# Performance work log

Measured on AMD Instinct MI355X. Metric: run time of the kernel, lower is better.

## Reference

```python
import jax, jax.numpy as jnp
import numpy as np

Q = 10000   # num_question
D = 64      # dim_s
M = 50      # size_m
B = 64      # batch
T = 512     # seq_len


def setup_inputs() -> dict:
    key = jax.random.key(0)
    ks = jax.random.split(key, 14)
    s = 1.0 / np.sqrt(D)
    inp = {
        "question": jax.random.randint(ks[0], (B, T), 0, Q, dtype=jnp.int32),
        "response": jax.random.randint(ks[1], (B, T), 0, 2, dtype=jnp.int32),
        "mask": jnp.ones((B, T), dtype=jnp.float32),
        "k_emb": jax.random.normal(ks[2], (Q, D), jnp.float32) * s,
        "v_emb": jax.random.normal(ks[3], (2 * Q, D), jnp.float32) * s,
        "Mk": jax.random.normal(ks[4], (M, D), jnp.float32) * np.sqrt(2.0 / D),
        "Mv0": jax.random.normal(ks[5], (M, D), jnp.float32) * np.sqrt(2.0 / D),
        "e_W": jax.random.normal(ks[6], (D, D), jnp.float32) * s,
        "e_b": jnp.zeros((D,), jnp.float32),
        "a_W": jax.random.normal(ks[7], (D, D), jnp.float32) * s,
        "a_b": jnp.zeros((D,), jnp.float32),
        "f_W": jax.random.normal(ks[8], (2 * D, D), jnp.float32) * (1.0 / np.sqrt(2 * D)),
        "f_b": jnp.zeros((D,), jnp.float32),
        "p_W": jax.random.normal(ks[9], (D, 1), jnp.float32) * s,
        "p_b": jnp.zeros((1,), jnp.float32),
    }
    return inp


def reference(question, response, mask, k_emb, v_emb, Mk, Mv0,
              e_W, e_b, a_W, a_b, f_W, f_b, p_W, p_b):
    num_q = k_emb.shape[0]
    bsz = question.shape[0]
    x = question + num_q * response                      # [B,T] combined ids
    k = k_emb[question]                                  # [B,T,D]
    v = v_emb[x]                                         # [B,T,D]
    w = jax.nn.softmax(k @ Mk.T, axis=-1)                # [B,T,M] read/write weights
    e = jax.nn.sigmoid(v @ e_W + e_b)                    # [B,T,D] erase
    a = jnp.tanh(v @ a_W + a_b)                          # [B,T,D] add

    def step(Mvt, inp):
        wt, et, at, mt = inp                             # [B,M],[B,D],[B,D],[B]
        Mvn = Mvt * (1.0 - wt[:, :, None] * et[:, None, :]) + wt[:, :, None] * at[:, None, :]
        Mvt = jnp.where(mt[:, None, None] == 1, Mvn, Mvt)
        return Mvt, Mvt

    Mv0b = jnp.broadcast_to(Mv0, (bsz,) + Mv0.shape)     # [B,M,D]
    xs = (jnp.swapaxes(w, 0, 1), jnp.swapaxes(e, 0, 1),
          jnp.swapaxes(a, 0, 1), mask.T)
    _, Mv_seq = jax.lax.scan(step, Mv0b, xs)             # [T,B,M,D] states after steps 0..T-1
    # read at step t (t>=1) uses state after step t-1
    Mv_read = jnp.swapaxes(Mv_seq[:-1], 0, 1)            # [B,T-1,M,D]
    read = jnp.einsum('btm,btmd->btd', w[:, 1:], Mv_read)
    f = jnp.tanh(jnp.concatenate([read, k[:, 1:]], axis=-1) @ f_W + f_b)
    p = (f @ p_W + p_b).squeeze(-1)                      # [B,T-1]
    return p
```

## Files before the change

kernel.cpp:

```cpp
#include <hip/hip_runtime.h>
#include <cstddef>

#define QN 10000
#define DD 64
#define MM 50
#define BB 64
#define TT 512
#define WPAD 52
#define MG 25

#define PIN(arr, n)                                        \
  _Pragma("unroll") for (int _p = 0; _p < (n); ++_p)       \
      asm volatile("" : "+v"((arr)[_p]));

__global__ __launch_bounds__(256) void kPre(
    const int* __restrict__ question, const int* __restrict__ response,
    const float* __restrict__ mask,
    const float* __restrict__ k_emb, const float* __restrict__ v_emb,
    const float* __restrict__ Mk,
    const float* __restrict__ e_W, const float* __restrict__ e_b,
    const float* __restrict__ a_W, const float* __restrict__ a_b,
    float* __restrict__ w_buf, float* __restrict__ e_buf,
    float* __restrict__ a_buf) {
  const int lane = (int)(threadIdx.x & 63);
  const int wslot = __builtin_amdgcn_readfirstlane((int)(threadIdx.x >> 6));
  const int gw = blockIdx.x * 4 + wslot;
  const int NW = gridDim.x * 4;
  const int third = NW / 3;
  if (gw >= 3 * third) return;
  const int role = gw / third;
  const int idx = gw - role * third;
  const int stride4 = third * 4;

  if (role == 0) {
    float mk[64];
    const int mrow = lane < MM ? lane : (MM - 1);
#pragma unroll
    for (int i = 0; i < 64; i += 4) {
      const float4 t4 = *(const float4*)(Mk + mrow * 64 + i);
      mk[i] = t4.x; mk[i + 1] = t4.y; mk[i + 2] = t4.z; mk[i + 3] = t4.w;
    }
    for (int base = idx * 4; base < BB * TT; base += stride4) {
      const int4 q4 = *(const int4*)(question + base);
      const float* __restrict__ kr0 = k_emb + (size_t)q4.x * 64;
      const float* __restrict__ kr1 = k_emb + (size_t)q4.y * 64;
      const float* __restrict__ kr2 = k_emb + (size_t)q4.z * 64;
      const float* __restrict__ kr3 = k_emb + (size_t)q4.w * 64;
      float l00=0.f,l01=0.f,l02=0.f,l03=0.f;
      float l10=0.f,l11=0.f,l12=0.f,l13=0.f;
      float l20=0.f,l21=0.f,l22=0.f,l23=0.f;
      float l30=0.f,l31=0.f,l32=0.f,l33=0.f;
#pragma unroll
      for (int i = 0; i < 64; i += 4) {
        const float4 k0 = *(const float4*)(kr0 + i);
        const float4 k1 = *(const float4*)(kr1 + i);
        const float4 k2 = *(const float4*)(kr2 + i);
        const float4 k3 = *(const float4*)(kr3 + i);
        l00 = fmaf(k0.x, mk[i], l00); l01 = fmaf(k0.y, mk[i+1], l01);
        l02 = fmaf(k0.z, mk[i+2], l02); l03 = fmaf(k0.w, mk[i+3], l03);
        l10 = fmaf(k1.x, mk[i], l10); l11 = fmaf(k1.y, mk[i+1], l11);
        l12 = fmaf(k1.z, mk[i+2], l12); l13 = fmaf(k1.w, mk[i+3], l13);
        l20 = fmaf(k2.x, mk[i], l20); l21 = fmaf(k2.y, mk[i+1], l21);
        l22 = fmaf(k2.z, mk[i+2], l22); l23 = fmaf(k2.w, mk[i+3], l23);
        l30 = fmaf(k3.x, mk[i], l30); l31 = fmaf(k3.y, mk[i+1], l31);
        l32 = fmaf(k3.z, mk[i+2], l32); l33 = fmaf(k3.w, mk[i+3], l33);
      }
      float lm[4];
      lm[0] = (l00 + l01) + (l02 + l03);
      lm[1] = (l10 + l11) + (l12 + l13);
      lm[2] = (l20 + l21) + (l22 + l23);
      lm[3] = (l30 + l31) + (l32 + l33);
#pragma unroll
      for (int r = 0; r < 4; ++r) {
        float lv = (lane < MM) ? lm[r] : -3.4e38f;
#pragma unroll
        for (int off = 32; off > 0; off >>= 1) lv = fmaxf(lv, __shfl_xor(lv, off));
        float pe = (lane < MM) ? __expf(lm[r] - lv) : 0.f;
        float ss = pe;
#pragma unroll
        for (int off = 32; off > 0; off >>= 1) ss += __shfl_xor(ss, off);
        if (lane < MM) w_buf[(size_t)(base + r) * WPAD + lane] = pe / ss;
      }
    }
  } else if (role == 1) {
    float ew[64];
#pragma unroll
    for (int i = 0; i < 64; ++i) ew[i] = e_W[i * 64 + lane];
    const float eb = e_b[lane];
    for (int base = idx * 4; base < BB * TT; base += stride4) {
      const int4 q4 = *(const int4*)(question + base);
      const int4 r4 = *(const int4*)(response + base);
      const float4 m4 = *(const float4*)(mask + base);
      const float* __restrict__ v0 = v_emb + ((size_t)q4.x + (size_t)QN * r4.x) * 64;
      const float* __restrict__ v1 = v_emb + ((size_t)q4.y + (size_t)QN * r4.y) * 64;
      const float* __restrict__ v2 = v_emb + ((size_t)q4.z + (size_t)QN * r4.z) * 64;
      const float* __restrict__ v3 = v_emb + ((size_t)q4.w + (size_t)QN * r4.w) * 64;
      float e00 = eb, e01 = 0.f, e10 = eb, e11 = 0.f;
      float e20 = eb, e21 = 0.f, e30 = eb, e31 = 0.f;
#pragma unroll
      for (int i = 0; i < 64; i += 2) {
        const float2 a0 = *(const float2*)(v0 + i);
        const float2 a1 = *(const float2*)(v1 + i);
        const float2 a2 = *(const float2*)(v2 + i);
        const float2 a3 = *(const float2*)(v3 + i);
        e00 = fmaf(a0.x, ew[i], e00); e01 = fmaf(a0.y, ew[i+1], e01);
        e10 = fmaf(a1.x, ew[i], e10); e11 = fmaf(a1.y, ew[i+1], e11);
        e20 = fmaf(a2.x, ew[i], e20); e21 = fmaf(a2.y, ew[i+1], e21);
        e30 = fmaf(a3.x, ew[i], e30); e31 = fmaf(a3.y, ew[i+1], e31);
      }
      const float mf0 = (m4.x == 1.0f) ? 1.0f : 0.0f;
      const float mf1 = (m4.y == 1.0f) ? 1.0f : 0.0f;
      const float mf2 = (m4.z == 1.0f) ? 1.0f : 0.0f;
      const float mf3 = (m4.w == 1.0f) ? 1.0f : 0.0f;
      e_buf[(size_t)(base + 0) * 64 + lane] = mf0 / (1.f + __expf(-(e00 + e01)));
      e_buf[(size_t)(base + 1) * 64 + lane] = mf1 / (1.f + __expf(-(e10 + e11)));
      e_buf[(size_t)(base + 2) * 64 + lane] = mf2 / (1.f + __expf(-(e20 + e21)));
      e_buf[(size_t)(base + 3) * 64 + lane] = mf3 / (1.f + __expf(-(e30 + e31)));
    }
  } else {
    float aw[64];
#pragma unroll
    for (int i = 0; i < 64; ++i) aw[i] = a_W[i * 64 + lane];
    const float ab = a_b[lane];
    for (int base = idx * 4; base < BB * TT; base += stride4) {
      const int4 q4 = *(const int4*)(question + base);
      const int4 r4 = *(const int4*)(response + base);
      const float4 m4 = *(const float4*)(mask + base);
      const float* __restrict__ v0 = v_emb + ((size_t)q4.x + (size_t)QN * r4.x) * 64;
      const float* __restrict__ v1 = v_emb + ((size_t)q4.y + (size_t)QN * r4.y) * 64;
      const float* __restrict__ v2 = v_emb + ((size_t)q4.z + (size_t)QN * r4.z) * 64;
      const float* __restrict__ v3 = v_emb + ((size_t)q4.w + (size_t)QN * r4.w) * 64;
      float a00 = ab, a01 = 0.f, a10 = ab, a11 = 0.f;
      float a20 = ab, a21 = 0.f, a30 = ab, a31 = 0.f;
#pragma unroll
      for (int i = 0; i < 64; i += 2) {
        const float2 x0 = *(const float2*)(v0 + i);
        const float2 x1 = *(const float2*)(v1 + i);
        const float2 x2 = *(const float2*)(v2 + i);
        const float2 x3 = *(const float2*)(v3 + i);
        a00 = fmaf(x0.x, aw[i], a00); a01 = fmaf(x0.y, aw[i+1], a01);
        a10 = fmaf(x1.x, aw[i], a10); a11 = fmaf(x1.y, aw[i+1], a11);
        a20 = fmaf(x2.x, aw[i], a20); a21 = fmaf(x2.y, aw[i+1], a21);
        a30 = fmaf(x3.x, aw[i], a30); a31 = fmaf(x3.y, aw[i+1], a31);
      }
      const float mf0 = (m4.x == 1.0f) ? 1.0f : 0.0f;
      const float mf1 = (m4.y == 1.0f) ? 1.0f : 0.0f;
      const float mf2 = (m4.z == 1.0f) ? 1.0f : 0.0f;
      const float mf3 = (m4.w == 1.0f) ? 1.0f : 0.0f;
      const float s0 = a00 + a01, s1 = a10 + a11, s2 = a20 + a21, s3 = a30 + a31;
      a_buf[(size_t)(base + 0) * 64 + lane] = mf0 * (1.f - 2.f / (__expf(2.f * s0) + 1.f));
      a_buf[(size_t)(base + 1) * 64 + lane] = mf1 * (1.f - 2.f / (__expf(2.f * s1) + 1.f));
      a_buf[(size_t)(base + 2) * 64 + lane] = mf2 * (1.f - 2.f / (__expf(2.f * s2) + 1.f));
      a_buf[(size_t)(base + 3) * 64 + lane] = mf3 * (1.f - 2.f / (__expf(2.f * s3) + 1.f));
    }
  }
}

#define STAGE_W(wl_row, rowbase)                                            \
  {                                                                         \
    const float* __restrict__ wsrc = w_buf + (rowbase) * WPAD;              \
    _Pragma("unroll") for (int k = 0; k < 13; ++k) {                        \
      const int idx = lane + k * 64;                            \
      const int row = idx / 52;                                             \
      const int col = idx - row * 52;                                       \
      (wl_row)[row * 56 + col + (col >= 25 ? 3 : 0)] = wsrc[idx];           \
    }                                                                       \
  }

#define LOAD_WM(wm, wl_row, j, g)                                           \
  const float* __restrict__ wj_##j = (wl_row) + (j) * 56 + (g) * 28;        \
  const float4 q0_##j = *(const float4*)(wj_##j + 0);                       \
  const float4 q1_##j = *(const float4*)(wj_##j + 4);                       \
  const float4 q2_##j = *(const float4*)(wj_##j + 8);                       \
  const float4 q3_##j = *(const float4*)(wj_##j + 12);                      \
  const float4 q4_##j = *(const float4*)(wj_##j + 16);                      \
  const float4 q5_##j = *(const float4*)(wj_##j + 20);                      \
  const float4 q6_##j = *(const float4*)(wj_##j + 24);                      \
  const float wm[MG] = {q0_##j.x, q0_##j.y, q0_##j.z, q0_##j.w,             \
                        q1_##j.x, q1_##j.y, q1_##j.z, q1_##j.w,             \
                        q2_##j.x, q2_##j.y, q2_##j.z, q2_##j.w,             \
                        q3_##j.x, q3_##j.y, q3_##j.z, q3_##j.w,             \
                        q4_##j.x, q4_##j.y, q4_##j.z, q4_##j.w,             \
                        q5_##j.x, q5_##j.y, q5_##j.z, q5_##j.w, q6_##j.x};

__global__ __launch_bounds__(256) void kA16(
    const float* __restrict__ w_buf, const float* __restrict__ e_buf,
    const float* __restrict__ a_buf, float* __restrict__ AB) {
  __shared__ float wl[4][16 * 56];
  const int lane = (int)(threadIdx.x & 63);
  const int wslot = __builtin_amdgcn_readfirstlane((int)(threadIdx.x >> 6));
  const int u2 = blockIdx.x * 4 + wslot;
  if (u2 >= BB * 32 * 2) return;
  const int g = u2 & 1;
  const int unit = u2 >> 1;
  const int b = unit >> 5;
  const int c = unit & 31;
  const size_t rowbase = (size_t)b * TT + c * 16;
  const size_t eb0 = rowbase * 64 + lane;

  float ev[16], av[16];
#pragma unroll
  for (int j = 0; j < 16; ++j) {
    ev[j] = e_buf[eb0 + (size_t)j * 64];
    av[j] = a_buf[eb0 + (size_t)j * 64];
  }
  STAGE_W(wl[wslot], rowbase)

  float Am[MG], Bm[MG];
#pragma unroll
  for (int m = 0; m < MG; ++m) { Am[m] = 1.f; Bm[m] = 0.f; }

#pragma unroll
  for (int j = 0; j < 16; ++j) {
    LOAD_WM(wm, wl[wslot], j, g)
#pragma unroll
    for (int m = 0; m < MG; ++m) {
      const float al = fmaf(-wm[m], ev[j], 1.0f);
      const float be = wm[m] * av[j];
      Am[m] *= al;
      Bm[m] = fmaf(Bm[m], al, be);
    }
  }
  float* __restrict__ abp = AB + (size_t)unit * 6400 + (g * MG) * 128 + lane * 2;
#pragma unroll
  for (int m = 0; m < MG; ++m) {
    float2 o; o.x = Am[m]; o.y = Bm[m];
    *(float2*)(abp + m * 128) = o;
  }
}

__global__ __launch_bounds__(256) void kB_entry(
    const float* __restrict__ AB, const float* __restrict__ Mv0,
    float* __restrict__ entry, int C) {
  const int NT = gridDim.x * 256;
  for (int idx = blockIdx.x * 256 + (int)threadIdx.x; idx < BB * MM * 64;
       idx += NT) {
    const int b = idx / (MM * 64);
    const int r = idx - b * (MM * 64);
    float s = Mv0[r];
    const float* __restrict__ abp = AB + (size_t)b * C * 6400 + (size_t)r * 2;
    float* __restrict__ ep = entry + (size_t)b * C * 3200 + r;
    if (C == 32) {
      float2 ab[32];
#pragma unroll
      for (int c = 0; c < 32; ++c)
        ab[c] = *(const float2*)(abp + (size_t)c * 6400);
#pragma unroll
      for (int c = 0; c < 32; ++c) {
        ep[(size_t)c * 3200] = s;
        s = fmaf(ab[c].x, s, ab[c].y);
      }
    } else {
      float2 cur = *(const float2*)(abp);
      for (int c = 0; c < C; ++c) {
        ep[(size_t)c * 3200] = s;
        float2 nxt; nxt.x = 1.f; nxt.y = 0.f;
        if (c + 1 < C) nxt = *(const float2*)(abp + (size_t)(c + 1) * 6400);
        s = fmaf(cur.x, s, cur.y);
        cur = nxt;
      }
    }
  }
}

__global__ __launch_bounds__(256) void kC16(
    const float* __restrict__ w_buf, const float* __restrict__ e_buf,
    const float* __restrict__ a_buf, const float* __restrict__ entry,
    float* __restrict__ read2) {
  __shared__ float wl[4][16 * 56];
  const int lane = (int)(threadIdx.x & 63);
  const int wslot = __builtin_amdgcn_readfirstlane((int)(threadIdx.x >> 6));
  const int u2 = blockIdx.x * 4 + wslot;
  if (u2 >= BB * 32 * 2) return;
  const int g = u2 & 1;
  const int unit = u2 >> 1;
  const int b = unit >> 5;
  const int c = unit & 31;
  const size_t RN = (size_t)BB * (TT - 1) * 64;
  const size_t rowbase = (size_t)b * TT + c * 16;
  const size_t eb0 = rowbase * 64 + lane;

  float ev[16], av[16];
#pragma unroll
  for (int j = 0; j < 16; ++j) {
    ev[j] = e_buf[eb0 + (size_t)j * 64];
    av[j] = a_buf[eb0 + (size_t)j * 64];
  }
  float s[MG];
  {
    const float* __restrict__ ep =
        entry + (size_t)unit * 3200 + (g * MG) * 64 + lane;
#pragma unroll
    for (int m = 0; m < MG; ++m) s[m] = ep[m * 64];
  }
  STAGE_W(wl[wslot], rowbase)

  const int t0 = c * 16;
  float* __restrict__ rb = read2 + (size_t)g * RN;
#pragma unroll
  for (int j = 0; j < 16; ++j) {
    const int t = t0 + j;
    LOAD_WM(wm, wl[wslot], j, g)
    if (t >= 1) {
      float a0 = 0.f, a1 = 0.f;
#pragma unroll
      for (int m = 0; m < MG - 1; m += 2) {
        a0 = fmaf(wm[m], s[m], a0);
        a1 = fmaf(wm[m + 1], s[m + 1], a1);
      }
      a0 = fmaf(wm[MG - 1], s[MG - 1], a0);
      rb[((size_t)b * (TT - 1) + (t - 1)) * 64 + lane] = a0 + a1;
    }
#pragma unroll
    for (int m = 0; m < MG; ++m)
      s[m] = fmaf(wm[m], fmaf(-s[m], ev[j], av[j]), s[m]);
  }
}

__global__ __launch_bounds__(256) void kA_chunk(
    const float* __restrict__ w_buf, const float* __restrict__ e_buf,
    const float* __restrict__ a_buf, float* __restrict__ AB, int logC, int L) {
  const int lane = (int)(threadIdx.x & 63);
  const int wslot = __builtin_amdgcn_readfirstlane((int)(threadIdx.x >> 6));
  const int NW = gridDim.x * 4;
  const int C = 1 << logC;
  for (int u2 = blockIdx.x * 4 + wslot; u2 < BB * C * 2; u2 += NW) {
    const int g = u2 & 1;
    const int unit = u2 >> 1;
    const int b = unit >> logC;
    const int c = unit & (C - 1);
    float Am[MG], Bm[MG];
#pragma unroll
    for (int m = 0; m < MG; ++m) { Am[m] = 1.f; Bm[m] = 0.f; }
    const size_t rowbase = (size_t)b * TT + c * L;
#pragma unroll 2
    for (int j = 0; j < L; ++j) {
      const size_t row = rowbase + j;
      const float ed = e_buf[row * 64 + lane];
      const float ad = a_buf[row * 64 + lane];
      const float* __restrict__ wr = w_buf + row * WPAD + g * MG;
#pragma unroll
      for (int m = 0; m < MG; ++m) {
        const float wm = wr[m];
        const float al = fmaf(-wm, ed, 1.0f);
        const float be = wm * ad;
        Am[m] *= al;
        Bm[m] = fmaf(Bm[m], al, be);
      }
    }
    float* __restrict__ abp = AB + (size_t)unit * 6400 + (g * MG) * 128 + lane * 2;
#pragma unroll
    for (int m = 0; m < MG; ++m) {
      float2 o; o.x = Am[m]; o.y = Bm[m];
      *(float2*)(abp + m * 128) = o;
    }
  }
}

__global__ __launch_bounds__(256) void kC_read(
    const float* __restrict__ w_buf, const float* __restrict__ e_buf,
    const float* __restrict__ a_buf, const float* __restrict__ entry,
    const float* __restrict__ Mv0, float* __restrict__ read2,
    int logC, int L, int use_mv0) {
  const int lane = (int)(threadIdx.x & 63);
  const int wslot = __builtin_amdgcn_readfirstlane((int)(threadIdx.x >> 6));
  const int NW = gridDim.x * 4;
  const int C = 1 << logC;
  const size_t RN = (size_t)BB * (TT - 1) * 64;
  for (int u2 = blockIdx.x * 4 + wslot; u2 < BB * C * 2; u2 += NW) {
    const int g = u2 & 1;
    const int unit = u2 >> 1;
    const int b = unit >> logC;
    const int c = unit & (C - 1);
    float s[MG];
    if (use_mv0) {
#pragma unroll
      for (int m = 0; m < MG; ++m) s[m] = Mv0[(g * MG + m) * 64 + lane];
    } else {
      const float* __restrict__ ep =
          entry + (size_t)unit * 3200 + (g * MG) * 64 + lane;
#pragma unroll
      for (int m = 0; m < MG; ++m) s[m] = ep[m * 64];
    }
    const int t0 = c * L;
    float* __restrict__ rb = read2 + (size_t)g * RN;
    for (int j = 0; j < L; ++j) {
      const int t = t0 + j;
      const size_t row = (size_t)b * TT + t;
      const float ed = e_buf[row * 64 + lane];
      const float ad = a_buf[row * 64 + lane];
      const float* __restrict__ wr = w_buf + row * WPAD + g * MG;
      if (t >= 1) {
        float a0 = 0.f, a1 = 0.f;
#pragma unroll
        for (int m = 0; m < MG - 1; m += 2) {
          a0 = fmaf(wr[m], s[m], a0);
          a1 = fmaf(wr[m + 1], s[m + 1], a1);
        }
        a0 = fmaf(wr[MG - 1], s[MG - 1], a0);
        rb[((size_t)b * (TT - 1) + (t - 1)) * 64 + lane] = a0 + a1;
      }
#pragma unroll
      for (int m = 0; m < MG; ++m)
        s[m] = fmaf(wr[m], fmaf(-s[m], ed, ad), s[m]);
    }
  }
}

__global__ __launch_bounds__(256) void k3_out(
    const int* __restrict__ question, const float* __restrict__ k_emb,
    const float* __restrict__ read2,
    const float* __restrict__ f_W, const float* __restrict__ f_b,
    const float* __restrict__ p_W, const float* __restrict__ p_b,
    float* __restrict__ out) {
  __shared__ float stg[4][2][64];
  const int lane = (int)(threadIdx.x & 63);
  const int ws = __builtin_amdgcn_readfirstlane((int)(threadIdx.x >> 6));
  const int NW = gridDim.x * 4;
  const size_t RN = (size_t)BB * (TT - 1) * 64;
  const int R = BB * (TT - 1);

  float fw[128];
#pragma unroll
  for (int i = 0; i < 128; ++i) fw[i] = f_W[i * 64 + lane];
  PIN(fw, 128)
  const float fb = f_b[lane];
  const float pw = p_W[lane];
  const float pb = p_b[0];

  int row = blockIdx.x * 4 + ws;
  float rd = 0.f, kl = 0.f;
  if (row < R) {
    rd = read2[(size_t)row * 64 + lane] + read2[RN + (size_t)row * 64 + lane];
    const int b = row / (TT - 1);
    const int tp = row - b * (TT - 1);
    const int qn = question[b * TT + tp + 1];
    kl = k_emb[(size_t)qn * 64 + lane];
  }
  while (row < R) {
    const int nrow = row + NW;
    float nrd = 0.f, nkl = 0.f;
    if (nrow < R) {
      nrd = read2[(size_t)nrow * 64 + lane] +
            read2[RN + (size_t)nrow * 64 + lane];
      const int nb = nrow / (TT - 1);
      const int ntp = nrow - nb * (TT - 1);
      const int nqn = question[nb * TT + ntp + 1];
      nkl = k_emb[(size_t)nqn * 64 + lane];
    }
    stg[ws][0][lane] = rd;
    stg[ws][1][lane] = kl;
    float f0 = fb, f1 = 0.f, f2 = 0.f, f3 = 0.f;
#pragma unroll
    for (int i = 0; i < 64; i += 4) {
      const float4 xv = *(const float4*)&stg[ws][0][i];
      f0 = fmaf(xv.x, fw[i], f0);
      f1 = fmaf(xv.y, fw[i + 1], f1);
      f2 = fmaf(xv.z, fw[i + 2], f2);
      f3 = fmaf(xv.w, fw[i + 3], f3);
    }
#pragma unroll
    for (int i = 0; i < 64; i += 4) {
      const float4 kv = *(const float4*)&stg[ws][1][i];
      f0 = fmaf(kv.x, fw[64 + i], f0);
      f1 = fmaf(kv.y, fw[64 + i + 1], f1);
      f2 = fmaf(kv.z, fw[64 + i + 2], f2);
      f3 = fmaf(kv.w, fw[64 + i + 3], f3);
    }
    const float f = (f0 + f1) + (f2 + f3);
    const float t2 = __expf(2.f * f);
    const float fv = 1.f - 2.f / (t2 + 1.f);
    float acc = fv * pw;
#pragma unroll
    for (int off = 32; off > 0; off >>= 1) acc += __shfl_xor(acc, off);
    if (lane == 0) out[row] = acc + pb;

    rd = nrd; kl = nkl; row = nrow;
  }
}

extern "C" void kernel_launch(void* const* d_in, const int* in_sizes, int n_in,
                              void* d_out, int out_size, void* d_ws, size_t ws_size,
                              hipStream_t stream) {
  const int*   question = (const int*)d_in[0];
  const int*   response = (const int*)d_in[1];
  const float* mask     = (const float*)d_in[2];
  const float* k_emb    = (const float*)d_in[3];
  const float* v_emb    = (const float*)d_in[4];
  const float* Mk       = (const float*)d_in[5];
  const float* Mv0      = (const float*)d_in[6];
  const float* e_W      = (const float*)d_in[7];
  const float* e_b      = (const float*)d_in[8];
  const float* a_W      = (const float*)d_in[9];
  const float* a_b      = (const float*)d_in[10];
  const float* f_W      = (const float*)d_in[11];
  const float* f_b      = (const float*)d_in[12];
  const float* p_W      = (const float*)d_in[13];
  const float* p_b      = (const float*)d_in[14];
  float* out = (float*)d_out;

  const size_t wN  = (size_t)BB * TT * WPAD;
  const size_t eN  = (size_t)BB * TT * 64;
  const size_t r2N = 2ull * BB * (TT - 1) * 64;
  float* ws = (float*)d_ws;
  float* w_buf  = ws;
  float* e_buf  = w_buf + wN;
  float* a_buf  = e_buf + eN;
  float* read2  = a_buf + eN;
  float* AB_arr = read2 + r2N;
  const size_t baseN = wN + 2 * eN + r2N;

  int C = 32, logC = 5;
  while (C >= 2) {
    const size_t need = (baseN + 9600ull * BB * C) * sizeof(float);
    if (need <= ws_size) break;
    C >>= 1; logC -= 1;
  }
  int useChunks = (C >= 2);
  if (!useChunks) { C = 1; logC = 0; }
  const int L = TT / C;
  float* entry = AB_arr + 6400ull * BB * C;

  hipLaunchKernelGGL(kPre, dim3(2048), dim3(256), 0, stream,
                     question, response, mask, k_emb, v_emb, Mk,
                     e_W, e_b, a_W, a_b, w_buf, e_buf, a_buf);

  if (C == 32) {
    hipLaunchKernelGGL(kA16, dim3(1024), dim3(256), 0, stream,
                       w_buf, e_buf, a_buf, AB_arr);
    hipLaunchKernelGGL(kB_entry, dim3((BB * MM * 64 + 255) / 256), dim3(256),
                       0, stream, AB_arr, Mv0, entry, C);
    hipLaunchKernelGGL(kC16, dim3(1024), dim3(256), 0, stream,
                       w_buf, e_buf, a_buf, entry, read2);
  } else {
    if (useChunks) {
      const int ublocksA = (BB * C * 2 + 3) / 4;
      hipLaunchKernelGGL(kA_chunk, dim3(ublocksA), dim3(256), 0, stream,
                         w_buf, e_buf, a_buf, AB_arr, logC, L);
      hipLaunchKernelGGL(kB_entry, dim3((BB * MM * 64 + 255) / 256), dim3(256),
                         0, stream, AB_arr, Mv0, entry, C);
    }
    const int ublocksC = (BB * C * 2 + 3) / 4;
    hipLaunchKernelGGL(kC_read, dim3(ublocksC), dim3(256), 0, stream,
                       w_buf, e_buf, a_buf, entry, Mv0, read2,
                       logC, L, useChunks ? 0 : 1);
  }

  hipLaunchKernelGGL(k3_out, dim3(1024), dim3(256), 0, stream,
                     question, k_emb, read2, f_W, f_b, p_W, p_b, out);
}
```

Before: 194.7 us.

## Split output projection across wave pairs and widen pre-kernel gathers to float4

In the pre-kernel erase/add paths, v_emb rows are now gathered with float4 loads instead of float2, which halves the number of load instructions. The output kernel now splits the 128-row f_W projection between two waves: one handles the read half and one the k_emb half. Their partial sums are combined through double-buffered shared memory with a block barrier every iteration. This halves per-wave weight registers, which may raise occupancy, but adds a __syncthreads per row and halves the rows processed per block.

After: 192.3 us. Within noise of the previous version (-1.3%).

```diff
diff --git a/kernel.cpp b/kernel.cpp
--- a/kernel.cpp
+++ b/kernel.cpp
@@ -98,15 +98,19 @@
       float e00 = eb, e01 = 0.f, e10 = eb, e11 = 0.f;
       float e20 = eb, e21 = 0.f, e30 = eb, e31 = 0.f;
 #pragma unroll
-      for (int i = 0; i < 64; i += 2) {
-        const float2 a0 = *(const float2*)(v0 + i);
-        const float2 a1 = *(const float2*)(v1 + i);
-        const float2 a2 = *(const float2*)(v2 + i);
-        const float2 a3 = *(const float2*)(v3 + i);
-        e00 = fmaf(a0.x, ew[i], e00); e01 = fmaf(a0.y, ew[i+1], e01);
-        e10 = fmaf(a1.x, ew[i], e10); e11 = fmaf(a1.y, ew[i+1], e11);
-        e20 = fmaf(a2.x, ew[i], e20); e21 = fmaf(a2.y, ew[i+1], e21);
-        e30 = fmaf(a3.x, ew[i], e30); e31 = fmaf(a3.y, ew[i+1], e31);
+      for (int i = 0; i < 64; i += 4) {
+        const float4 a0 = *(const float4*)(v0 + i);
+        const float4 a1 = *(const float4*)(v1 + i);
+        const float4 a2 = *(const float4*)(v2 + i);
+        const float4 a3 = *(const float4*)(v3 + i);
+        e00 = fmaf(a0.x, ew[i], e00);     e01 = fmaf(a0.y, ew[i + 1], e01);
+        e00 = fmaf(a0.z, ew[i + 2], e00); e01 = fmaf(a0.w, ew[i + 3], e01);
+        e10 = fmaf(a1.x, ew[i], e10);     e11 = fmaf(a1.y, ew[i + 1], e11);
+        e10 = fmaf(a1.z, ew[i + 2], e10); e11 = fmaf(a1.w, ew[i + 3], e11);
+        e20 = fmaf(a2.x, ew[i], e20);     e21 = fmaf(a2.y, ew[i + 1], e21);
+        e20 = fmaf(a2.z, ew[i + 2], e20); e21 = fmaf(a2.w, ew[i + 3], e21);
+        e30 = fmaf(a3.x, ew[i], e30);     e31 = fmaf(a3.y, ew[i + 1], e31);
+        e30 = fmaf(a3.z, ew[i + 2], e30); e31 = fmaf(a3.w, ew[i + 3], e31);
       }
       const float mf0 = (m4.x == 1.0f) ? 1.0f : 0.0f;
       const float mf1 = (m4.y == 1.0f) ? 1.0f : 0.0f;
@@ -133,15 +137,19 @@
       float a00 = ab, a01 = 0.f, a10 = ab, a11 = 0.f;
       float a20 = ab, a21 = 0.f, a30 = ab, a31 = 0.f;
 #pragma unroll
-      for (int i = 0; i < 64; i += 2) {
-        const float2 x0 = *(const float2*)(v0 + i);
-        const float2 x1 = *(const float2*)(v1 + i);
-        const float2 x2 = *(const float2*)(v2 + i);
-        const float2 x3 = *(const float2*)(v3 + i);
-        a00 = fmaf(x0.x, aw[i], a00); a01 = fmaf(x0.y, aw[i+1], a01);
-        a10 = fmaf(x1.x, aw[i], a10); a11 = fmaf(x1.y, aw[i+1], a11);
-        a20 = fmaf(x2.x, aw[i], a20); a21 = fmaf(x2.y, aw[i+1], a21);
-        a30 = fmaf(x3.x, aw[i], a30); a31 = fmaf(x3.y, aw[i+1], a31);
+      for (int i = 0; i < 64; i += 4) {
+        const float4 x0 = *(const float4*)(v0 + i);
+        const float4 x1 = *(const float4*)(v1 + i);
+        const float4 x2 = *(const float4*)(v2 + i);
+        const float4 x3 = *(const float4*)(v3 + i);
+        a00 = fmaf(x0.x, aw[i], a00);     a01 = fmaf(x0.y, aw[i + 1], a01);
+        a00 = fmaf(x0.z, aw[i + 2], a00); a01 = fmaf(x0.w, aw[i + 3], a01);
+        a10 = fmaf(x1.x, aw[i], a10);     a11 = fmaf(x1.y, aw[i + 1], a11);
+        a10 = fmaf(x1.z, aw[i + 2], a10); a11 = fmaf(x1.w, aw[i + 3], a11);
+        a20 = fmaf(x2.x, aw[i], a20);     a21 = fmaf(x2.y, aw[i + 1], a21);
+        a20 = fmaf(x2.z, aw[i + 2], a20); a21 = fmaf(x2.w, aw[i + 3], a21);
+        a30 = fmaf(x3.x, aw[i], a30);     a31 = fmaf(x3.y, aw[i + 1], a31);
+        a30 = fmaf(x3.z, aw[i + 2], a30); a31 = fmaf(x3.w, aw[i + 3], a31);
       }
       const float mf0 = (m4.x == 1.0f) ? 1.0f : 0.0f;
       const float mf1 = (m4.y == 1.0f) ? 1.0f : 0.0f;
@@ -413,69 +421,79 @@
     const float* __restrict__ f_W, const float* __restrict__ f_b,
     const float* __restrict__ p_W, const float* __restrict__ p_b,
     float* __restrict__ out) {
-  __shared__ float stg[4][2][64];
+  __shared__ float pbuf[2][2][64];
+  __shared__ float stg[4][64];
   const int lane = (int)(threadIdx.x & 63);
   const int ws = __builtin_amdgcn_readfirstlane((int)(threadIdx.x >> 6));
-  const int NW = gridDim.x * 4;
+  const int pair = ws >> 1;
+  const int g = ws & 1;
+  const int NP = gridDim.x * 2;
   const size_t RN = (size_t)BB * (TT - 1) * 64;
   const int R = BB * (TT - 1);
-
-  float fw[128];
-#pragma unroll
-  for (int i = 0; i < 128; ++i) fw[i] = f_W[i * 64 + lane];
-  PIN(fw, 128)
+  const int iters = (R + NP - 1) / NP;
+
+  float fw[64];
+#pragma unroll
+  for (int i = 0; i < 64; ++i) fw[i] = f_W[(g * 64 + i) * 64 + lane];
+  PIN(fw, 64)
   const float fb = f_b[lane];
   const float pw = p_W[lane];
   const float pb = p_b[0];
 
-  int row = blockIdx.x * 4 + ws;
-  float rd = 0.f, kl = 0.f;
+  int row = blockIdx.x * 2 + pair;
+  float cur = 0.f;
   if (row < R) {
-    rd = read2[(size_t)row * 64 + lane] + read2[RN + (size_t)row * 64 + lane];
-    const int b = row / (TT - 1);
-    const int tp = row - b * (TT - 1);
-    const int qn = question[b * TT + tp + 1];
-    kl = k_emb[(size_t)qn * 64 + lane];
-  }
-  while (row < R) {
-    const int nrow = row + NW;
-    float nrd = 0.f, nkl = 0.f;
+    if (g == 0) {
+      cur = read2[(size_t)row * 64 + lane] + read2[RN + (size_t)row * 64 + lane];
+    } else {
+      const int b = row / (TT - 1);
+      const int tp = row - b * (TT - 1);
+      const int qn = question[b * TT + tp + 1];
+      cur = k_emb[(size_t)qn * 64 + lane];
+    }
+  }
+  for (int it = 0; it < iters; ++it) {
+    const int nrow = row + NP;
+    float nxt = 0.f;
     if (nrow < R) {
-      nrd = read2[(size_t)nrow * 64 + lane] +
-            read2[RN + (size_t)nrow * 64 + lane];
-      const int nb = nrow / (TT - 1);
-      const int ntp = nrow - nb * (TT - 1);
-      const int nqn = question[nb * TT + ntp + 1];
-      nkl = k_emb[(size_t)nqn * 64 + lane];
-    }
-    stg[ws][0][lane] = rd;
-    stg[ws][1][lane] = kl;
-    float f0 = fb, f1 = 0.f, f2 = 0.f, f3 = 0.f;
-#pragma unroll
-    for (int i = 0; i < 64; i += 4) {
-      const float4 xv = *(const float4*)&stg[ws][0][i];
-      f0 = fmaf(xv.x, fw[i], f0);
-      f1 = fmaf(xv.y, fw[i + 1], f1);
-      f2 = fmaf(xv.z, fw[i + 2], f2);
-      f3 = fmaf(xv.w, fw[i + 3], f3);
-    }
-#pragma unroll
-    for (int i = 0; i < 64; i += 4) {
-      const float4 kv = *(const float4*)&stg[ws][1][i];
-      f0 = fmaf(kv.x, fw[64 + i], f0);
-      f1 = fmaf(kv.y, fw[64 + i + 1], f1);
-      f2 = fmaf(kv.z, fw[64 + i + 2], f2);
-      f3 = fmaf(kv.w, fw[64 + i + 3], f3);
-    }
-    const float f = (f0 + f1) + (f2 + f3);
-    const float t2 = __expf(2.f * f);
-    const float fv = 1.f - 2.f / (t2 + 1.f);
-    float acc = fv * pw;
-#pragma unroll
-    for (int off = 32; off > 0; off >>= 1) acc += __shfl_xor(acc, off);
-    if (lane == 0) out[row] = acc + pb;
-
-    rd = nrd; kl = nkl; row = nrow;
+      if (g == 0) {
+        nxt = read2[(size_t)nrow * 64 + lane] +
+              read2[RN + (size_t)nrow * 64 + lane];
+      } else {
+        const int nb = nrow / (TT - 1);
+        const int ntp = nrow - nb * (TT - 1);
+        const int nqn = question[nb * TT + ntp + 1];
+        nxt = k_emb[(size_t)nqn * 64 + lane];
+      }
+    }
+    const bool active = (row < R);
+    float partial = 0.f;
+    if (active) {
+      stg[ws][lane] = cur;
+      float f0 = (g == 0) ? fb : 0.f, f1 = 0.f, f2 = 0.f, f3 = 0.f;
+#pragma unroll
+      for (int i = 0; i < 64; i += 4) {
+        const float4 xv = *(const float4*)&stg[ws][i];
+        f0 = fmaf(xv.x, fw[i], f0);
+        f1 = fmaf(xv.y, fw[i + 1], f1);
+        f2 = fmaf(xv.z, fw[i + 2], f2);
+        f3 = fmaf(xv.w, fw[i + 3], f3);
+      }
+      partial = (f0 + f1) + (f2 + f3);
+    }
+    const int pr = it & 1;
+    if (active && g == 1) pbuf[pr][pair][lane] = partial;
+    __syncthreads();
+    if (active && g == 0) {
+      const float f = partial + pbuf[pr][pair][lane];
+      const float t2 = __expf(2.f * f);
+      const float fv = 1.f - 2.f / (t2 + 1.f);
+      float acc = fv * pw;
+#pragma unroll
+      for (int off = 32; off > 0; off >>= 1) acc += __shfl_xor(acc, off);
+      if (lane == 0) out[row] = acc + pb;
+    }
+    row = nrow; cur = nxt;
   }
 }
 
```
